# Optimization experiments

Hardware: AMD Instinct MI355X
Metric: run time of the kernel (lower is better)

The kernel has to match this reference:

```python
import jax, jax.numpy as jnp
import numpy as np

MASK_VALUE = -10000.0  # module uses masked_fill(-10000), not -inf


def setup_inputs() -> dict:
    key = jax.random.key(0)
    kq, kk, kv = jax.random.split(key, 3)
    B, H, S, D = 2, 16, 2048, 64
    return {
        "query_states": jax.random.normal(kq, (B, H, S, D), dtype=jnp.float32),
        "key_states": jax.random.normal(kk, (B, H, S, D), dtype=jnp.float32),
        "value_states": jax.random.normal(kv, (B, H, S, D), dtype=jnp.float32),
    }


def reference(query_states, key_states, value_states):
    B, H, S, D = query_states.shape
    kv_len = key_states.shape[-2]
    scale = 1.0 / jnp.sqrt(jnp.asarray(D, dtype=query_states.dtype))
    # [B,H,S,kv] scores
    scores = jnp.einsum("bhqd,bhkd->bhqk", query_states, key_states) * scale
    # causal mask: positions strictly above the diagonal are masked (triu diag=1)
    causal = jnp.arange(kv_len)[None, :] > jnp.arange(S)[:, None]  # [S, kv]
    scores = jnp.where(causal[None, None], MASK_VALUE, scores)
    # softmax in float32 (module upcasts), then back to input dtype
    probs = jax.nn.softmax(scores.astype(jnp.float32), axis=-1).astype(query_states.dtype)
    return jnp.einsum("bhqk,bhkd->bhqd", probs, value_states)
```

## Files before the change

kernel.cpp:

```cpp
#include <hip/hip_runtime.h>


#define S_LEN 2048
#define D_DIM 64
#define QSCALE 0.1803368867f
#define CSHIFT 23.0831206542f
#define BHSTR 131072

typedef __attribute__((ext_vector_type(8))) short short8;
typedef __attribute__((ext_vector_type(4))) short short4v;
typedef __attribute__((ext_vector_type(4))) float float4v;

typedef const __attribute__((address_space(1))) void cg_void;
typedef __attribute__((address_space(3))) void lds_void;

__device__ __forceinline__ short f2bf(float x) {
    union { float f; unsigned u; } c; c.f = x;
    unsigned u = c.u + 0x7fffu + ((c.u >> 16) & 1u);
    return (short)(u >> 16);
}

#if __has_builtin(__builtin_amdgcn_mfma_f32_16x16x16_bf16)
__device__ __forceinline__ float4v mfma16(short4v a, short4v b, float4v c) {
    return __builtin_amdgcn_mfma_f32_16x16x16_bf16(a, b, c, 0, 0, 0);
}
#elif __has_builtin(__builtin_amdgcn_mfma_f32_16x16x16bf16_1k)
__device__ __forceinline__ float4v mfma16(short4v a, short4v b, float4v c) {
    return __builtin_amdgcn_mfma_f32_16x16x16bf16_1k(a, b, c, 0, 0, 0);
}
#else
__device__ __forceinline__ float4v mfma16(short4v a, short4v b, float4v c) {
    float4v d;
    asm("v_mfma_f32_16x16x16_bf16 %0, %1, %2, %3"
        : "=v"(d) : "v"(a), "v"(b), "0"(c));
    return d;
}
#endif

#define PVS 80
__global__ __launch_bounds__(256, 4)
void prep(const float* __restrict__ K, const float* __restrict__ V,
          short* __restrict__ Kbf, short* __restrict__ Vt) {
    __shared__ __align__(16) short Vl[D_DIM * PVS];
    const int tid = threadIdx.x;
    const int st  = blockIdx.x;
    const int bh  = blockIdx.y;
    const size_t base = ((size_t)bh * S_LEN + st * 64) * D_DIM;

    #pragma unroll
    for (int i = 0; i < 4; ++i) {
        const int e = (i * 256 + tid) * 4;
        const int kv = e >> 6, d0 = e & 63;
        float4v k4 = *(const float4v*)(K + base + e);
        short4v ks = { f2bf(k4.x), f2bf(k4.y), f2bf(k4.z), f2bf(k4.w) };
        *(short4v*)(Kbf + base + e) = ks;
        float4v v4 = *(const float4v*)(V + base + e);
        Vl[(d0 + 0) * PVS + kv] = f2bf(v4.x);
        Vl[(d0 + 1) * PVS + kv] = f2bf(v4.y);
        Vl[(d0 + 2) * PVS + kv] = f2bf(v4.z);
        Vl[(d0 + 3) * PVS + kv] = f2bf(v4.w);
    }
    __syncthreads();
    const int d = tid >> 2, c = tid & 3;
    short8 a = *(const short8*)&Vl[d * PVS + c * 16];
    short8 b = *(const short8*)&Vl[d * PVS + c * 16 + 8];
    short* dst = Vt + (size_t)bh * BHSTR + (size_t)d * S_LEN + st * 64 + c * 16;
    *(short8*)dst = a;
    *(short8*)(dst + 8) = b;
}

__global__ __launch_bounds__(128, 2)
void fa_fwd6(const float* __restrict__ Q, const short* __restrict__ Kbf,
             const short* __restrict__ Vt, float* __restrict__ O) {
    __shared__ __align__(16) short SB[18432];

    const int tid  = threadIdx.x;
    const int w    = tid >> 6;
    const int lane = tid & 63;
    const int l15  = lane & 15;
    const int quad = lane >> 4;

    const int bh  = blockIdx.y;
    const int blk = gridDim.x - 1 - blockIdx.x;
    const int q0  = blk * 64;

    const float* Qb  = Q + (size_t)bh * S_LEN * D_DIM;
    const short* KbB = Kbf + (size_t)bh * BHSTR;
    const short* VtB = Vt  + (size_t)bh * BHSTR;
    float*       Ob  = O + (size_t)bh * S_LEN * D_DIM;

    const short* gsrc[9]; int gcoef[9];
    #pragma unroll
    for (int i = 0; i < 9; ++i) {
        const int s = i * 128 + tid;
        if (s < 576) {
            const int row = s / 9, j = s - row * 9;
            const int j8 = (j == 8) ? 0 : j;
            gsrc[i] = KbB + row * 64 + j8 * 8;
            gcoef[i] = 4096;
        } else {
            const int ss = s - 576;
            const int row = ss / 9, j = ss - row * 9;
            const int j8 = (j == 8) ? 7 : j;
            gsrc[i] = VtB + (size_t)row * S_LEN + j8 * 8;
            gcoef[i] = 64;
        }
    }

    short8 qfrag[2][2];
    #pragma unroll
    for (int qt = 0; qt < 2; ++qt) {
        const float* qp = Qb + (size_t)(q0 + (w * 2 + qt) * 16 + l15) * D_DIM;
        #pragma unroll
        for (int c = 0; c < 2; ++c) {
            const int d0 = c * 32 + quad * 8;
            float4v a = *(const float4v*)(qp + d0);
            float4v b = *(const float4v*)(qp + d0 + 4);
            qfrag[qt][c][0] = f2bf(a.x * QSCALE); qfrag[qt][c][1] = f2bf(a.y * QSCALE);
            qfrag[qt][c][2] = f2bf(a.z * QSCALE); qfrag[qt][c][3] = f2bf(a.w * QSCALE);
            qfrag[qt][c][4] = f2bf(b.x * QSCALE); qfrag[qt][c][5] = f2bf(b.y * QSCALE);
            qfrag[qt][c][6] = f2bf(b.z * QSCALE); qfrag[qt][c][7] = f2bf(b.w * QSCALE);
        }
    }

    float l_lane[2] = {0.f, 0.f};
    float4v o_acc[2][4];
    #pragma unroll
    for (int qt = 0; qt < 2; ++qt)
        #pragma unroll
        for (int td = 0; td < 4; ++td) o_acc[qt][td] = (float4v)0.0f;

    const int n_tiles = blk + 1;

    #pragma unroll
    for (int i = 0; i < 9; ++i)
        __builtin_amdgcn_global_load_lds(
            (cg_void*)gsrc[i],
            (lds_void*)&SB[i * 1024 + w * 512],
            16, 0, 0);
    __syncthreads();

    for (int t = 0; t < n_tiles; ++t) {
        const int cur = (t & 1) * 9216;

        if (t + 1 < n_tiles) {
            const int nxt = 9216 - cur;
            #pragma unroll
            for (int i = 0; i < 9; ++i) {
                gsrc[i] += gcoef[i];
                __builtin_amdgcn_global_load_lds(
                    (cg_void*)gsrc[i],
                    (lds_void*)&SB[nxt + i * 1024 + w * 512],
                    16, 0, 0);
            }
        }

        const short* Ks = SB + cur;
        const short* Vs = SB + cur + 4608;

        float4v sc[2][4];
        #pragma unroll
        for (int tt = 0; tt < 4; ++tt) {
            const short* kr = &Ks[(tt * 16 + l15) * 72 + quad * 8];
            short8 k0 = *(const short8*)(kr);
            short8 k1 = *(const short8*)(kr + 32);
            #pragma unroll
            for (int qt = 0; qt < 2; ++qt) {
                float4v acc = (float4v)0.0f;
                acc = __builtin_amdgcn_mfma_f32_16x16x32_bf16(k0, qfrag[qt][0], acc, 0, 0, 0);
                acc = __builtin_amdgcn_mfma_f32_16x16x32_bf16(k1, qfrag[qt][1], acc, 0, 0, 0);
                sc[qt][tt] = acc;
            }
        }

        if (t == blk) {
            #pragma unroll
            for (int qt = 0; qt < 2; ++qt) {
                const int qrow = q0 + (w * 2 + qt) * 16 + l15;
                #pragma unroll
                for (int tt = 0; tt < 4; ++tt) {
                    const int kv = t * 64 + tt * 16 + quad * 4;
                    #pragma unroll
                    for (int r = 0; r < 4; ++r)
                        if (kv + r > qrow) sc[qt][tt][r] = -3.0e38f;
                }
            }
        }

        short4v pb[2][4];
        #pragma unroll
        for (int qt = 0; qt < 2; ++qt)
            #pragma unroll
            for (int tt = 0; tt < 4; ++tt) {
                #pragma unroll
                for (int r = 0; r < 4; ++r) {
                    float p = __builtin_amdgcn_exp2f(sc[qt][tt][r] - CSHIFT);
                    sc[qt][tt][r] = p;
                    l_lane[qt] += p;
                }
                pb[qt][tt] = short4v{ f2bf(sc[qt][tt][0]), f2bf(sc[qt][tt][1]),
                                      f2bf(sc[qt][tt][2]), f2bf(sc[qt][tt][3]) };
            }

        #pragma unroll
        for (int td = 0; td < 4; ++td) {
            const short* vr = &Vs[(td * 16 + l15) * 72 + quad * 4];
            #pragma unroll
            for (int tt = 0; tt < 4; ++tt) {
                short4v va = *(const short4v*)(vr + tt * 16);
                #pragma unroll
                for (int qt = 0; qt < 2; ++qt)
                    o_acc[qt][td] = mfma16(va, pb[qt][tt], o_acc[qt][td]);
            }
        }

        __syncthreads();
    }

    #pragma unroll
    for (int qt = 0; qt < 2; ++qt) {
        float l = l_lane[qt];
        l += __shfl_xor(l, 16);
        l += __shfl_xor(l, 32);
        const float inv = 1.0f / l;
        const int qrow = q0 + (w * 2 + qt) * 16 + l15;
        float* op = Ob + (size_t)qrow * D_DIM + quad * 4;
        #pragma unroll
        for (int td = 0; td < 4; ++td) {
            float4v st = { o_acc[qt][td][0] * inv, o_acc[qt][td][1] * inv,
                           o_acc[qt][td][2] * inv, o_acc[qt][td][3] * inv };
            *(float4v*)(op + td * 16) = st;
        }
    }
}

#define KSTR 72
__global__ __launch_bounds__(256, 2)
void fa_fwd_fb(const float* __restrict__ Q, const float* __restrict__ K,
               const float* __restrict__ V, float* __restrict__ O) {
    __shared__ __align__(16) short Ksf[64 * KSTR];
    __shared__ __align__(16) short Vsf[D_DIM * KSTR];
    __shared__ __align__(16) short Psf[4 * 16 * KSTR];

    const int tid = threadIdx.x, w = tid >> 6, lane = tid & 63;
    const int l15 = lane & 15, quad = lane >> 4;
    const int bh = blockIdx.y, blk = gridDim.x - 1 - blockIdx.x, q0 = blk * 64;
    const float* Qb = Q + (size_t)bh * S_LEN * D_DIM;
    const float* Kb = K + (size_t)bh * S_LEN * D_DIM;
    const float* Vb = V + (size_t)bh * S_LEN * D_DIM;
    float* Ob = O + (size_t)bh * S_LEN * D_DIM;

    short8 qfrag[2];
    {
        const float* qp = Qb + (size_t)(q0 + w * 16 + l15) * D_DIM;
        #pragma unroll
        for (int c = 0; c < 2; ++c) {
            const int d0 = c * 32 + quad * 8;
            float4v a = *(const float4v*)(qp + d0);
            float4v b = *(const float4v*)(qp + d0 + 4);
            qfrag[c][0] = f2bf(a.x * 0.125f); qfrag[c][1] = f2bf(a.y * 0.125f);
            qfrag[c][2] = f2bf(a.z * 0.125f); qfrag[c][3] = f2bf(a.w * 0.125f);
            qfrag[c][4] = f2bf(b.x * 0.125f); qfrag[c][5] = f2bf(b.y * 0.125f);
            qfrag[c][6] = f2bf(b.z * 0.125f); qfrag[c][7] = f2bf(b.w * 0.125f);
        }
    }
    const int crow0 = q0 + w * 16 + quad * 4;
    float m_run[4], l_run[4];
    float4v o_acc[4];
    #pragma unroll
    for (int r = 0; r < 4; ++r) { m_run[r] = -1e30f; l_run[r] = 0.0f; }
    #pragma unroll
    for (int td = 0; td < 4; ++td) o_acc[td] = (float4v)0.0f;
    short* Pw = Psf + w * 16 * KSTR;
    const int n_tiles = blk + 1;

    for (int t = 0; t < n_tiles; ++t) {
        const int kv0 = t * 64;
        __syncthreads();
        #pragma unroll
        for (int i = 0; i < 4; ++i) {
            const int slot = tid + i * 256;
            const int row = slot >> 4, d4 = (slot & 15) << 2;
            float4v k4 = *(const float4v*)(Kb + (size_t)(kv0 + row) * D_DIM + d4);
            short4v ks = { f2bf(k4.x), f2bf(k4.y), f2bf(k4.z), f2bf(k4.w) };
            *(short4v*)&Ksf[row * KSTR + d4] = ks;
            float4v v4 = *(const float4v*)(Vb + (size_t)(kv0 + row) * D_DIM + d4);
            Vsf[(d4 + 0) * KSTR + row] = f2bf(v4.x);
            Vsf[(d4 + 1) * KSTR + row] = f2bf(v4.y);
            Vsf[(d4 + 2) * KSTR + row] = f2bf(v4.z);
            Vsf[(d4 + 3) * KSTR + row] = f2bf(v4.w);
        }
        __syncthreads();
        float4v sc[4];
        #pragma unroll
        for (int tt = 0; tt < 4; ++tt) {
            float4v acc = (float4v)0.0f;
            #pragma unroll
            for (int c = 0; c < 2; ++c) {
                short8 bf = *(const short8*)&Ksf[(tt * 16 + l15) * KSTR + c * 32 + quad * 8];
                acc = __builtin_amdgcn_mfma_f32_16x16x32_bf16(qfrag[c], bf, acc, 0, 0, 0);
            }
            sc[tt] = acc;
        }
        if (t == n_tiles - 1) {
            #pragma unroll
            for (int tt = 0; tt < 4; ++tt) {
                const int col = kv0 + tt * 16 + l15;
                #pragma unroll
                for (int r = 0; r < 4; ++r)
                    if (col > crow0 + r) sc[tt][r] = -1e30f;
            }
        }
        #pragma unroll
        for (int r = 0; r < 4; ++r) {
            float mx = fmaxf(fmaxf(sc[0][r], sc[1][r]), fmaxf(sc[2][r], sc[3][r]));
            #pragma unroll
            for (int off = 1; off <= 8; off <<= 1)
                mx = fmaxf(mx, __shfl_xor(mx, off));
            const float m_new = fmaxf(m_run[r], mx);
            const float alpha = __expf(m_run[r] - m_new);
            m_run[r] = m_new;
            float rs = 0.0f;
            #pragma unroll
            for (int tt = 0; tt < 4; ++tt) {
                float pv = __expf(sc[tt][r] - m_new);
                sc[tt][r] = pv; rs += pv;
            }
            #pragma unroll
            for (int off = 1; off <= 8; off <<= 1)
                rs += __shfl_xor(rs, off);
            l_run[r] = l_run[r] * alpha + rs;
            #pragma unroll
            for (int td = 0; td < 4; ++td) o_acc[td][r] *= alpha;
        }
        #pragma unroll
        for (int tt = 0; tt < 4; ++tt)
            #pragma unroll
            for (int r = 0; r < 4; ++r)
                Pw[(quad * 4 + r) * KSTR + tt * 16 + l15] = f2bf(sc[tt][r]);
        short8 pf[2];
        #pragma unroll
        for (int c = 0; c < 2; ++c)
            pf[c] = *(const short8*)&Pw[l15 * KSTR + c * 32 + quad * 8];
        #pragma unroll
        for (int td = 0; td < 4; ++td)
            #pragma unroll
            for (int c = 0; c < 2; ++c) {
                short8 bv = *(const short8*)&Vsf[(td * 16 + l15) * KSTR + c * 32 + quad * 8];
                o_acc[td] = __builtin_amdgcn_mfma_f32_16x16x32_bf16(pf[c], bv, o_acc[td], 0, 0, 0);
            }
    }
    #pragma unroll
    for (int td = 0; td < 4; ++td)
        #pragma unroll
        for (int r = 0; r < 4; ++r)
            Ob[(size_t)(crow0 + r) * D_DIM + td * 16 + l15] = o_acc[td][r] / l_run[r];
}

extern "C" void kernel_launch(void* const* d_in, const int* in_sizes, int n_in,
                              void* d_out, int out_size, void* d_ws, size_t ws_size,
                              hipStream_t stream) {
    const float* Q = (const float*)d_in[0];
    const float* K = (const float*)d_in[1];
    const float* V = (const float*)d_in[2];
    float* O = (float*)d_out;
    const size_t elems = (size_t)2 * 16 * S_LEN * D_DIM;
    if (ws_size >= 2 * elems * sizeof(short)) {
        short* Kbf = (short*)d_ws;
        short* Vt  = Kbf + elems;
        prep<<<dim3(32, 32), 256, 0, stream>>>(K, V, Kbf, Vt);
        fa_fwd6<<<dim3(32, 32), 128, 0, stream>>>(Q, Kbf, Vt, O);
    } else {
        fa_fwd_fb<<<dim3(32, 32), 256, 0, stream>>>(Q, K, V, O);
    }
}
```

Before: 145.7 us.

## Split long causal query blocks across two workgroups and combine partial results

Adds a split-KV flash-attention kernel. Each of the upper 16 query blocks per head is handled by two workgroups, one covering KV tiles 0-15 and one covering the rest, so the causal triangle is spread more evenly over 48 workgroups per head instead of 32 of very unequal length. Partial outputs and row sums go to workspace, and a new combine kernel adds them and normalizes; this works without max rescaling because softmax uses a fixed shift. The new kernel uses single-buffered LDS with synchronous loads to allow higher occupancy, which removes the previous load/compute overlap. It also adds a third launch plus extra workspace traffic.

```diff
diff --git a/kernel.cpp b/kernel.cpp
--- a/kernel.cpp
+++ b/kernel.cpp
@@ -67,6 +67,188 @@
     short* dst = Vt + (size_t)bh * BHSTR + (size_t)d * S_LEN + st * 64 + c * 16;
     *(short8*)dst = a;
     *(short8*)(dst + 8) = b;
+}
+
+__global__ __launch_bounds__(128, 4)
+void fa_fwd8(const float* __restrict__ Q, const short* __restrict__ Kbf,
+             const short* __restrict__ Vt, float* __restrict__ O,
+             float* __restrict__ OA, float* __restrict__ lab) {
+    __shared__ __align__(16) short SB[9216];
+
+    const int tid  = threadIdx.x;
+    const int w    = tid >> 6;
+    const int lane = tid & 63;
+    const int l15  = lane & 15;
+    const int quad = lane >> 4;
+
+    const int bh  = blockIdx.y;
+    const int xid = blockIdx.x;
+    int i, t0, t1, mode;
+    if (xid < 16)      { i = 16 + xid;  t0 = 0;  t1 = 16;    mode = 1; }
+    else if (xid < 32) { i = 31 - xid;  t0 = 0;  t1 = i + 1; mode = 0; }
+    else               { i = 63 - xid;  t0 = 16; t1 = i + 1; mode = 2; }
+    const int q0 = i * 64;
+
+    const float* Qb  = Q + (size_t)bh * S_LEN * D_DIM;
+    const short* KbB = Kbf + (size_t)bh * BHSTR;
+    const short* VtB = Vt  + (size_t)bh * BHSTR;
+    float*       Ob  = O + (size_t)bh * S_LEN * D_DIM;
+
+    const short* gsrc[9]; int gcoef[9];
+    #pragma unroll
+    for (int ii = 0; ii < 9; ++ii) {
+        const int s = ii * 128 + tid;
+        if (s < 576) {
+            const int row = s / 9, j = s - row * 9;
+            const int j8 = (j == 8) ? 0 : j;
+            gsrc[ii] = KbB + row * 64 + j8 * 8;
+            gcoef[ii] = 4096;
+        } else {
+            const int ss = s - 576;
+            const int row = ss / 9, j = ss - row * 9;
+            const int j8 = (j == 8) ? 7 : j;
+            gsrc[ii] = VtB + (size_t)row * S_LEN + j8 * 8;
+            gcoef[ii] = 64;
+        }
+    }
+
+    short8 qfrag[2][2];
+    #pragma unroll
+    for (int qt = 0; qt < 2; ++qt) {
+        const float* qp = Qb + (size_t)(q0 + (w * 2 + qt) * 16 + l15) * D_DIM;
+        #pragma unroll
+        for (int c = 0; c < 2; ++c) {
+            const int d0 = c * 32 + quad * 8;
+            float4v a = *(const float4v*)(qp + d0);
+            float4v b = *(const float4v*)(qp + d0 + 4);
+            qfrag[qt][c][0] = f2bf(a.x * QSCALE); qfrag[qt][c][1] = f2bf(a.y * QSCALE);
+            qfrag[qt][c][2] = f2bf(a.z * QSCALE); qfrag[qt][c][3] = f2bf(a.w * QSCALE);
+            qfrag[qt][c][4] = f2bf(b.x * QSCALE); qfrag[qt][c][5] = f2bf(b.y * QSCALE);
+            qfrag[qt][c][6] = f2bf(b.z * QSCALE); qfrag[qt][c][7] = f2bf(b.w * QSCALE);
+        }
+    }
+
+    float l_lane[2] = {0.f, 0.f};
+    float4v o_acc[2][4];
+    #pragma unroll
+    for (int qt = 0; qt < 2; ++qt)
+        #pragma unroll
+        for (int td = 0; td < 4; ++td) o_acc[qt][td] = (float4v)0.0f;
+
+    const short* Ks = SB;
+    const short* Vs = SB + 4608;
+
+    for (int t = t0; t < t1; ++t) {
+        __syncthreads();
+        #pragma unroll
+        for (int ii = 0; ii < 9; ++ii)
+            __builtin_amdgcn_global_load_lds(
+                (cg_void*)(gsrc[ii] + (size_t)t * gcoef[ii]),
+                (lds_void*)&SB[ii * 1024 + w * 512],
+                16, 0, 0);
+        __syncthreads();
+
+        float4v sc[2][4];
+        #pragma unroll
+        for (int tt = 0; tt < 4; ++tt) {
+            const short* kr = &Ks[(tt * 16 + l15) * 72 + quad * 8];
+            short8 k0 = *(const short8*)(kr);
+            short8 k1 = *(const short8*)(kr + 32);
+            #pragma unroll
+            for (int qt = 0; qt < 2; ++qt) {
+                float4v acc = (float4v)0.0f;
+                acc = __builtin_amdgcn_mfma_f32_16x16x32_bf16(k0, qfrag[qt][0], acc, 0, 0, 0);
+                acc = __builtin_amdgcn_mfma_f32_16x16x32_bf16(k1, qfrag[qt][1], acc, 0, 0, 0);
+                sc[qt][tt] = acc;
+            }
+        }
+
+        if (t == i) {
+            #pragma unroll
+            for (int qt = 0; qt < 2; ++qt) {
+                const int qrow = q0 + (w * 2 + qt) * 16 + l15;
+                #pragma unroll
+                for (int tt = 0; tt < 4; ++tt) {
+                    const int kv = t * 64 + tt * 16 + quad * 4;
+                    #pragma unroll
+                    for (int r = 0; r < 4; ++r)
+                        if (kv + r > qrow) sc[qt][tt][r] = -3.0e38f;
+                }
+            }
+        }
+
+        short4v pb[2][4];
+        #pragma unroll
+        for (int qt = 0; qt < 2; ++qt)
+            #pragma unroll
+            for (int tt = 0; tt < 4; ++tt) {
+                #pragma unroll
+                for (int r = 0; r < 4; ++r) {
+                    float p = __builtin_amdgcn_exp2f(sc[qt][tt][r] - CSHIFT);
+                    sc[qt][tt][r] = p;
+                    l_lane[qt] += p;
+                }
+                pb[qt][tt] = short4v{ f2bf(sc[qt][tt][0]), f2bf(sc[qt][tt][1]),
+                                      f2bf(sc[qt][tt][2]), f2bf(sc[qt][tt][3]) };
+            }
+
+        #pragma unroll
+        for (int td = 0; td < 4; ++td) {
+            const short* vr = &Vs[(td * 16 + l15) * 72 + quad * 4];
+            #pragma unroll
+            for (int tt = 0; tt < 4; ++tt) {
+                short4v va = *(const short4v*)(vr + tt * 16);
+                #pragma unroll
+                for (int qt = 0; qt < 2; ++qt)
+                    o_acc[qt][td] = mfma16(va, pb[qt][tt], o_acc[qt][td]);
+            }
+        }
+    }
+
+    #pragma unroll
+    for (int qt = 0; qt < 2; ++qt) {
+        float l = l_lane[qt];
+        l += __shfl_xor(l, 16);
+        l += __shfl_xor(l, 32);
+        const int qrow = q0 + (w * 2 + qt) * 16 + l15;
+        if (mode == 0) {
+            const float inv = 1.0f / l;
+            float* op = Ob + (size_t)qrow * D_DIM + quad * 4;
+            #pragma unroll
+            for (int td = 0; td < 4; ++td) {
+                float4v st = { o_acc[qt][td][0] * inv, o_acc[qt][td][1] * inv,
+                               o_acc[qt][td][2] * inv, o_acc[qt][td][3] * inv };
+                *(float4v*)(op + td * 16) = st;
+            }
+        } else {
+            const int rloc = qrow - 1024;
+            float* op = (mode == 2)
+                ? (Ob + (size_t)qrow * D_DIM + quad * 4)
+                : (OA + ((size_t)bh * 1024 + rloc) * D_DIM + quad * 4);
+            #pragma unroll
+            for (int td = 0; td < 4; ++td)
+                *(float4v*)(op + td * 16) = o_acc[qt][td];
+            if (quad == 0)
+                lab[(mode == 1 ? 0 : 32768) + bh * 1024 + rloc] = l;
+        }
+    }
+}
+
+__global__ __launch_bounds__(256, 4)
+void combine(float* __restrict__ O, const float* __restrict__ OA,
+             const float* __restrict__ lab) {
+    const int bh = blockIdx.y;
+    const int g  = blockIdx.x * 256 + threadIdx.x;
+    const int row = g >> 4;
+    const int d4  = (g & 15) * 4;
+    const float l = lab[bh * 1024 + row] + lab[32768 + bh * 1024 + row];
+    const float inv = 1.0f / l;
+    float4v a = *(const float4v*)(OA + ((size_t)bh * 1024 + row) * D_DIM + d4);
+    float* op = O + ((size_t)bh * S_LEN + 1024 + row) * D_DIM + d4;
+    float4v o = *(const float4v*)op;
+    float4v r = { (o[0] + a[0]) * inv, (o[1] + a[1]) * inv,
+                  (o[2] + a[2]) * inv, (o[3] + a[3]) * inv };
+    *(float4v*)op = r;
 }
 
 __global__ __launch_bounds__(128, 2)
@@ -135,26 +317,20 @@
     #pragma unroll
     for (int i = 0; i < 9; ++i)
         __builtin_amdgcn_global_load_lds(
-            (cg_void*)gsrc[i],
-            (lds_void*)&SB[i * 1024 + w * 512],
-            16, 0, 0);
+            (cg_void*)gsrc[i], (lds_void*)&SB[i * 1024 + w * 512], 16, 0, 0);
     __syncthreads();
 
     for (int t = 0; t < n_tiles; ++t) {
         const int cur = (t & 1) * 9216;
-
         if (t + 1 < n_tiles) {
             const int nxt = 9216 - cur;
             #pragma unroll
             for (int i = 0; i < 9; ++i) {
                 gsrc[i] += gcoef[i];
                 __builtin_amdgcn_global_load_lds(
-                    (cg_void*)gsrc[i],
-                    (lds_void*)&SB[nxt + i * 1024 + w * 512],
-                    16, 0, 0);
-            }
-        }
-
+                    (cg_void*)gsrc[i], (lds_void*)&SB[nxt + i * 1024 + w * 512], 16, 0, 0);
+            }
+        }
         const short* Ks = SB + cur;
         const short* Vs = SB + cur + 4608;
 
@@ -213,7 +389,6 @@
                     o_acc[qt][td] = mfma16(va, pb[qt][tt], o_acc[qt][td]);
             }
         }
-
         __syncthreads();
     }
 
@@ -365,7 +540,17 @@
     const float* V = (const float*)d_in[2];
     float* O = (float*)d_out;
     const size_t elems = (size_t)2 * 16 * S_LEN * D_DIM;
-    if (ws_size >= 2 * elems * sizeof(short)) {
+    const size_t needKV = 2 * elems * sizeof(short);
+    const size_t needSplit = needKV + 8388608 + 262144;
+    if (ws_size >= needSplit) {
+        short* Kbf = (short*)d_ws;
+        short* Vt  = Kbf + elems;
+        float* OA  = (float*)(Vt + elems);
+        float* lab = OA + 2097152;
+        prep<<<dim3(32, 32), 256, 0, stream>>>(K, V, Kbf, Vt);
+        fa_fwd8<<<dim3(48, 32), 128, 0, stream>>>(Q, Kbf, Vt, O, OA, lab);
+        combine<<<dim3(64, 32), 256, 0, stream>>>(O, OA, lab);
+    } else if (ws_size >= needKV) {
         short* Kbf = (short*)d_ws;
         short* Vt  = Kbf + elems;
         prep<<<dim3(32, 32), 256, 0, stream>>>(K, V, Kbf, Vt);
```

After: 154.4 us. 6.0% more time.
